# Kernel tuning notes

Measured on AMD Instinct MI355X. Metric: run time of the kernel, lower is better.

Reference implementation:

```python
import jax, jax.numpy as jnp
import numpy as np
import math

N = 50000
E = 1600000
A = 100          # num_atoms
H = 64           # hidden_dim / node_dim
L = 5            # num_layers
NB = 8           # num_basis
LMAX = 2
CUTOFF = 5.0


def setup_inputs() -> dict:
    key = jax.random.key(0)
    ks = jax.random.split(key, 32)
    s = 0.05
    inp = {
        'atomic_numbers': jax.random.randint(ks[0], (N,), 0, A),
        'pos': jax.random.normal(ks[1], (N, 3), jnp.float32) * 2.0,
        'edge_index': jax.random.randint(ks[2], (2, E), 0, N),
        # GaussianBasis widths
        'widths': jnp.ones((NB,), jnp.float32) * 0.5,
        # node embedding
        'embed': jax.random.normal(ks[3], (A, H), jnp.float32),
        # per-layer params, stacked on leading layer dim
        'rad_w1': jax.random.normal(ks[4], (L, NB, H), jnp.float32) * s,
        'rad_b1': jnp.zeros((L, H), jnp.float32),
        'rad_w2': jax.random.normal(ks[5], (L, H, H * (LMAX + 1)), jnp.float32) * s,
        'rad_b2': jnp.zeros((L, H * (LMAX + 1)), jnp.float32),
        'self_w': jax.random.normal(ks[6], (L, H, H), jnp.float32) * s,
        'self_b': jnp.zeros((L, H), jnp.float32),
        'proj_w': jax.random.normal(ks[7], (L, 2 * H, H), jnp.float32) * s,
        'proj_b': jnp.zeros((L, H), jnp.float32),
        'mlp_w1': jax.random.normal(ks[8], (L, H, 2 * H), jnp.float32) * s,
        'mlp_b1': jnp.zeros((L, 2 * H), jnp.float32),
        'mlp_w2': jax.random.normal(ks[9], (L, 2 * H, H), jnp.float32) * s,
        'mlp_b2': jnp.zeros((L, H), jnp.float32),
        'ln_g': jnp.ones((L, H), jnp.float32),
        'ln_b': jnp.zeros((L, H), jnp.float32),
        # readout MLP
        'ro_w1': jax.random.normal(ks[10], (H, H), jnp.float32) * s,
        'ro_b1': jnp.zeros((H,), jnp.float32),
        'ro_w2': jax.random.normal(ks[11], (H, H // 2), jnp.float32) * s,
        'ro_b2': jnp.zeros((H // 2,), jnp.float32),
        'ro_w3': jax.random.normal(ks[12], (H // 2, 1), jnp.float32) * s,
        'ro_b3': jnp.zeros((1,), jnp.float32),
        # per-species reference energies
        'atomic_e': jax.random.normal(ks[13], (A, 1), jnp.float32) * s,
    }
    return inp


def _layer_norm(x, g, b, eps=1e-5):
    mu = jnp.mean(x, axis=-1, keepdims=True)
    var = jnp.var(x, axis=-1, keepdims=True)
    return (x - mu) * jax.lax.rsqrt(var + eps) * g + b


def _spherical_harmonics(edge_vec):
    # real SH up to lmax=2, [E, 9] (computed for fidelity; unused by conv math)
    r = jnp.clip(jnp.linalg.norm(edge_vec, axis=-1), 1e-8, None)
    x, y, z = edge_vec[:, 0] / r, edge_vec[:, 1] / r, edge_vec[:, 2] / r
    x2, y2, z2 = x * x, y * y, z * z
    return jnp.stack([
        jnp.full_like(x, 0.28209479177387814),
        -0.4886025119029199 * y, 0.4886025119029199 * z, -0.4886025119029199 * x,
        1.0925484305920792 * x * y, -1.0925484305920792 * y * z,
        0.94617469575756 * z2 - 0.31539156525252 * (x2 + y2),
        -1.0925484305920792 * x * z, 0.5462742152960396 * (x2 - y2),
    ], axis=-1)


def _forward(atomic_numbers, pos, edge_index, widths, embed,
             rad_w1, rad_b1, rad_w2, rad_b2, self_w, self_b, proj_w, proj_b,
             mlp_w1, mlp_b1, mlp_w2, mlp_b2, ln_g, ln_b,
             ro_w1, ro_b1, ro_w2, ro_b2, ro_w3, ro_b3, atomic_e):
    n = pos.shape[0]
    row, col = edge_index[0], edge_index[1]
    edge_vec = pos[col] - pos[row]                          # [E,3]
    edge_len = jnp.linalg.norm(edge_vec, axis=-1, keepdims=True)  # [E,1]

    # GaussianBasis
    xr = edge_len / CUTOFF
    cut = 0.5 * (jnp.cos(xr * math.pi) + 1.0)
    cut = cut * (edge_len < CUTOFF).astype(jnp.float32)     # [E,1]
    centers = jnp.linspace(0.0, CUTOFF, NB)
    diff = edge_len - centers                               # [E,NB]
    edge_rbf = jnp.exp(-0.5 * (diff / jnp.clip(widths, 0.1, None)) ** 2) * cut

    edge_sh = _spherical_harmonics(edge_vec)  # computed but unused, as in source

    feats = embed[atomic_numbers]                           # [N,H]
    for i in range(L):
        # radial net -> per-edge weights [E, H*(lmax+1)]
        w = jax.nn.silu(edge_rbf @ rad_w1[i] + rad_b1[i]) @ rad_w2[i] + rad_b2[i]
        # messages: node_j[:,:,None] * w.view(E,H,lmax+1) summed over last dim
        # == node_j * w.reshape(E,H,lmax+1).sum(-1)
        wsum = w.reshape(-1, H, LMAX + 1).sum(axis=-1)      # [E,H]
        messages = feats[col] * wsum                        # gather + multiply
        agg = jax.ops.segment_sum(messages, row, num_segments=n)  # scatter-add
        self_out = feats @ self_w[i] + self_b[i]
        conv_out = jnp.concatenate([self_out, agg], axis=-1) @ proj_w[i] + proj_b[i]
        upd = jax.nn.silu(conv_out @ mlp_w1[i] + mlp_b1[i]) @ mlp_w2[i] + mlp_b2[i]
        feats = _layer_norm(feats + upd, ln_g[i], ln_b[i])

    h = jax.nn.silu(feats @ ro_w1 + ro_b1)
    h = jax.nn.silu(h @ ro_w2 + ro_b2)
    atomic_energies = h @ ro_w3 + ro_b3                     # [N,1]
    atomic_energies = atomic_energies + atomic_e[atomic_numbers]
    return atomic_energies.sum()                            # batch=None path


def reference(atomic_numbers, pos, edge_index, widths, embed,
              rad_w1, rad_b1, rad_w2, rad_b2, self_w, self_b, proj_w, proj_b,
              mlp_w1, mlp_b1, mlp_w2, mlp_b2, ln_g, ln_b,
              ro_w1, ro_b1, ro_w2, ro_b2, ro_w3, ro_b3, atomic_e):
    return _forward(atomic_numbers, pos, edge_index, widths, embed,
                    rad_w1, rad_b1, rad_w2, rad_b2, self_w, self_b, proj_w, proj_b,
                    mlp_w1, mlp_b1, mlp_w2, mlp_b2, ln_g, ln_b,
                    ro_w1, ro_b1, ro_w2, ro_b2, ro_w3, ro_b3, atomic_e)
```

## Files before the change

### kernel.cpp

```cpp
#include <hip/hip_runtime.h>
#include <hip/hip_fp16.h>
#include <math.h>

constexpr int N_NODES = 50000;
constexpr int N_EDGES = 1600000;
constexpr int HDIM    = 64;
constexpr int NLAYER  = 5;
constexpr int NBASIS  = 8;
constexpr int TLUT    = 256;
constexpr float CUT_R = 5.0f;
constexpr float PI_F  = 3.14159265358979f;

constexpr int NBKT = 196;
constexpr int BCAP = 9216;
constexpr int TILE = 2048;

typedef __attribute__((ext_vector_type(8))) short short8;
typedef __attribute__((ext_vector_type(4))) float f32x4;
#define MFMA16 __builtin_amdgcn_mfma_f32_16x16x32_bf16

__device__ __forceinline__ float siluf(float x) { return x / (1.0f + __expf(-x)); }

__device__ __forceinline__ unsigned int f2bf(float x) {
    unsigned int b = __float_as_uint(x);
    return (b + 0x7fffu + ((b >> 16) & 1u)) >> 16;
}
__device__ __forceinline__ float bf_lo(unsigned int u) { return __uint_as_float(u << 16); }
__device__ __forceinline__ float bf_hi(unsigned int u) { return __uint_as_float(u & 0xffff0000u); }

__device__ __forceinline__ unsigned int f2e5(float x) {
    unsigned short b = __half_as_ushort(__float2half(x));
    return ((unsigned int)b + 0x7Fu + ((b >> 8) & 1u)) >> 8;
}

__device__ __forceinline__ __half2 u2h2(unsigned int u) {
    union { unsigned int u; __half2 h; } x; x.u = u; return x.h;
}
__device__ __forceinline__ unsigned int h2u(__half2 h) {
    union { __half2 h; unsigned int u; } x; x.h = h; return x.u;
}

__device__ __forceinline__ int blockScan256Excl(int cv, int tid, int* wtot) {
    int v = cv;
    int lane = tid & 63;
    #pragma unroll
    for (int off = 1; off < 64; off <<= 1) {
        int t = __shfl_up(v, off, 64);
        if (lane >= off) v += t;
    }
    if (lane == 63) wtot[tid >> 6] = v;
    __syncthreads();
    int pre = 0;
    #pragma unroll
    for (int w = 0; w < 4; ++w)
        if (w < (tid >> 6)) pre += wtot[w];
    __syncthreads();
    return v + pre - cv;
}


__global__ void k_embed(const int* __restrict__ an, const float* __restrict__ embed,
                        unsigned short* __restrict__ featsbf,
                        unsigned char* __restrict__ featsf8) {
    int i = blockIdx.x * blockDim.x + threadIdx.x;
    if (i >= N_NODES * HDIM) return;
    int node = i >> 6, h = i & 63;
    float v = embed[an[node] * HDIM + h];
    featsbf[i] = (unsigned short)f2bf(v);
    featsf8[i] = (unsigned char)f2e5(v);
}

__global__ void k_edge(const int* __restrict__ row, const int* __restrict__ col,
                       const float* __restrict__ pos,
                       unsigned int* __restrict__ rec4, unsigned char* __restrict__ bkt) {
    int e = blockIdx.x * blockDim.x + threadIdx.x;
    if (e >= N_EDGES) return;
    int r = row[e], c = col[e];
    float dx = pos[c * 3 + 0] - pos[r * 3 + 0];
    float dy = pos[c * 3 + 1] - pos[r * 3 + 1];
    float dz = pos[c * 3 + 2] - pos[r * 3 + 2];
    float len = sqrtf(dx * dx + dy * dy + dz * dz);
    float t = len * ((float)(TLUT - 1) / CUT_R);
    t = fminf(t, (float)(TLUT - 1));
    unsigned int nn = (unsigned int)(t + 0.5f);
    if (nn > TLUT - 1) nn = TLUT - 1;
    rec4[e] = ((unsigned int)c << 16) | (nn << 8) | ((unsigned int)r & 255u);
    bkt[e]  = (unsigned char)(r >> 8);
}

__global__ __launch_bounds__(256) void k_binA(const unsigned int* __restrict__ rec4,
                                              const unsigned char* __restrict__ bkt,
                                              int* __restrict__ btail,
                                              unsigned int* __restrict__ binned) {
    __shared__ unsigned int ent[TILE];
    __shared__ short bb[TILE];
    __shared__ unsigned int sorted[TILE];
    __shared__ short sortedB[TILE];
    __shared__ int cnt[256], cnt2[256], base[256], gbase[256];
    __shared__ int wtot[4];
    const int tid = threadIdx.x;
    const int t0  = blockIdx.x * TILE;
    const int nv  = min(TILE, N_EDGES - t0);

    cnt[tid] = 0;
    __syncthreads();

    #pragma unroll
    for (int i = 0; i < TILE / 256; ++i) {
        int idx = i * 256 + tid;
        if (idx < nv) {
            ent[idx] = rec4[t0 + idx];
            int b = bkt[t0 + idx];
            bb[idx] = (short)b;
            atomicAdd(&cnt[b], 1);
        }
    }
    __syncthreads();
    int cv = cnt[tid];
    int excl = blockScan256Excl(cv, tid, wtot);
    base[tid] = excl;
    if (tid < NBKT && cv > 0) gbase[tid] = atomicAdd(&btail[tid], cv);
    cnt2[tid] = excl;
    __syncthreads();
    #pragma unroll
    for (int i = 0; i < TILE / 256; ++i) {
        int idx = i * 256 + tid;
        if (idx < nv) {
            int b = bb[idx];
            int p = atomicAdd(&cnt2[b], 1);
            sorted[p]  = ent[idx];
            sortedB[p] = (short)b;
        }
    }
    __syncthreads();
    for (int s = tid; s < nv; s += 256) {
        int b = sortedB[s];
        binned[(size_t)b * BCAP + gbase[b] + (s - base[b])] = sorted[s];
    }
}

__global__ void k_scanB(const int* __restrict__ btail, int* __restrict__ bbase) {
    __shared__ int wtot[4];
    int t = threadIdx.x;
    int v = (t < NBKT) ? btail[t] : 0;
    int excl = blockScan256Excl(v, t, wtot);
    if (t < NBKT) bbase[t] = excl;
}

__global__ __launch_bounds__(256) void k_binB(const unsigned int* __restrict__ binned,
                                              const int* __restrict__ btail,
                                              const int* __restrict__ bbase,
                                              int* __restrict__ starts,
                                              unsigned int* __restrict__ erec) {
    __shared__ int hist[256];
    __shared__ int cur[256];
    __shared__ int wtot[4];
    const int b = blockIdx.x;
    const int node0 = b << 8;
    const int t = threadIdx.x;
    hist[t] = 0;
    __syncthreads();
    const int cnt = btail[b];
    const unsigned int* src = binned + (size_t)b * BCAP;
    for (int s = t; s < cnt; s += 256)
        atomicAdd(&hist[src[s] & 255u], 1);
    __syncthreads();
    int h = hist[t];
    int excl = bbase[b] + blockScan256Excl(h, t, wtot);
    int n = node0 + t;
    if (n < N_NODES) starts[n] = excl;
    if (b == 0 && t == 0) starts[N_NODES] = N_EDGES;
    cur[t] = excl;
    __syncthreads();
    for (int s = t; s < cnt; s += 256) {
        unsigned int p = src[s];
        int pp = atomicAdd(&cur[p & 255u], 1);
        erec[pp] = p;
    }
}

__global__ void k_prep(const float* __restrict__ rad_w2, const float* __restrict__ self_w,
                       const float* __restrict__ proj_w,
                       const float* __restrict__ rad_b2, const float* __restrict__ self_b,
                       const float* __restrict__ proj_b,
                       float* __restrict__ W2s, float* __restrict__ Wsp,
                       float* __restrict__ b2s, float* __restrict__ bsp) {
    int i = blockIdx.x * blockDim.x + threadIdx.x;
    if (i < NLAYER * HDIM * HDIM) {
        int l = i / (HDIM * HDIM); int rem = i % (HDIM * HDIM);
        int k = rem / HDIM; int h = rem % HDIM;
        const float* w = rad_w2 + ((size_t)l * HDIM + k) * (HDIM * 3) + h * 3;
        W2s[i] = w[0] + w[1] + w[2];
        const float* sw = self_w + ((size_t)l * HDIM + k) * HDIM;
        const float* pw = proj_w + (size_t)l * 2 * HDIM * HDIM;
        float acc = 0.f;
        for (int m = 0; m < HDIM; ++m) acc += sw[m] * pw[m * HDIM + h];
        Wsp[i] = acc;
    } else {
        int i2 = i - NLAYER * HDIM * HDIM;
        if (i2 >= NLAYER * HDIM) return;
        int l = i2 / HDIM, h = i2 % HDIM;
        const float* rb2 = rad_b2 + l * HDIM * 3 + h * 3;
        b2s[i2] = rb2[0] + rb2[1] + rb2[2];
        float acc = proj_b[l * HDIM + h];
        const float* pw = proj_w + (size_t)l * 2 * HDIM * HDIM;
        const float* sb = self_b + l * HDIM;
        for (int m = 0; m < HDIM; ++m) acc += sb[m] * pw[m * HDIM + h];
        bsp[i2] = acc;
    }
}

__global__ void k_wtr(const float* __restrict__ Wsp, const float* __restrict__ proj_w,
                      const float* __restrict__ mlp_w1, const float* __restrict__ mlp_w2,
                      const float* __restrict__ ro_w1, const float* __restrict__ ro_w2,
                      unsigned short* __restrict__ WspT, unsigned short* __restrict__ PbT,
                      unsigned short* __restrict__ W1T, unsigned short* __restrict__ W2T,
                      unsigned short* __restrict__ Ro1T, unsigned short* __restrict__ Ro2T) {
    int i = blockIdx.x * blockDim.x + threadIdx.x;
    if (i < NLAYER * 24576) {
        int l = i / 24576, off = i % 24576;
        if (off < 4096) {
            int n = off >> 6, k = off & 63;
            WspT[(size_t)l * 4096 + off] = (unsigned short)f2bf(Wsp[(size_t)l * 4096 + k * 64 + n]);
        } else if (off < 8192) {
            int o = off - 4096; int n = o >> 6, k = o & 63;
            PbT[(size_t)l * 4096 + o] =
                (unsigned short)f2bf(proj_w[(size_t)l * 8192 + (64 + k) * 64 + n]);
        } else if (off < 16384) {
            int o = off - 8192; int n = o >> 6, k = o & 63;
            W1T[(size_t)l * 8192 + o] = (unsigned short)f2bf(mlp_w1[(size_t)l * 8192 + k * 128 + n]);
        } else {
            int o = off - 16384; int n = o >> 7, k = o & 127;
            W2T[(size_t)l * 8192 + o] = (unsigned short)f2bf(mlp_w2[(size_t)l * 8192 + k * 64 + n]);
        }
    } else {
        int i2 = i - NLAYER * 24576;
        if (i2 >= 6144) return;
        if (i2 < 4096) {
            int n = i2 >> 6, k = i2 & 63;
            Ro1T[i2] = (unsigned short)f2bf(ro_w1[k * 64 + n]);
        } else {
            int o = i2 - 4096; int n = o >> 6, k = o & 63;
            Ro2T[o] = (unsigned short)f2bf(ro_w2[k * 32 + n]);
        }
    }
}

__global__ void k_lut(const float* __restrict__ widths, const float* __restrict__ rad_w1,
                      const float* __restrict__ rad_b1, const float* __restrict__ W2s,
                      const float* __restrict__ b2s, unsigned short* __restrict__ lutH) {
    int bid = blockIdx.x;
    int l = bid / TLUT, t = bid % TLUT;
    int h = threadIdx.x;
    __shared__ float h1s[HDIM];
    float len = (float)t * (CUT_R / (float)(TLUT - 1));
    float cut = 0.0f;
    if (len < CUT_R) cut = 0.5f * (cosf(len * (PI_F / CUT_R)) + 1.0f);
    float acc = rad_b1[l * HDIM + h];
    for (int b = 0; b < NBASIS; ++b) {
        float wb = fmaxf(widths[b], 0.1f);
        float center = (float)b * (CUT_R / (float)(NBASIS - 1));
        float d = (len - center) / wb;
        float rbf = __expf(-0.5f * d * d) * cut;
        acc += rbf * rad_w1[(l * NBASIS + b) * HDIM + h];
    }
    h1s[h] = siluf(acc);
    __syncthreads();
    float o = b2s[l * HDIM + h];
    const float* w2 = W2s + (size_t)l * HDIM * HDIM;
    for (int k = 0; k < HDIM; ++k) o += h1s[k] * w2[k * HDIM + h];
    int m = h & 7;
    int pos = (h & ~7) | (m & 4) | ((m & 1) << 1) | ((m >> 1) & 1);
    lutH[(size_t)bid * HDIM + pos] = __half_as_ushort(__float2half(o));
}


__global__ __launch_bounds__(256) void k_agg(const uint2* __restrict__ featsf8_2,
                                             const uint4* __restrict__ lutH4_l,
                                             const int* __restrict__ starts,
                                             const unsigned int* __restrict__ erec,
                                             uint4* __restrict__ aggbf4) {
    int wid  = (blockIdx.x * blockDim.x + threadIdx.x) >> 6;
    int lane = threadIdx.x & 63;
    int slot = lane >> 3;
    int j    = lane & 7;
    if (wid >= N_NODES) return;
    int e0 = starts[wid], e1 = starts[wid + 1];
    __half2 a02 = u2h2(0u), a13 = u2h2(0u), a46 = u2h2(0u), a57 = u2h2(0u);
    #pragma unroll 2
    for (int e = e0 + slot; e < e1; e += 8) {
        unsigned int rec = erec[e];
        int c  = rec >> 16;
        int i0 = (rec >> 8) & 255;
        uint4 qw = lutH4_l[i0 * 8 + j];
        uint2 fb = featsf8_2[(size_t)c * 8 + j];
        a02 = __hfma2(u2h2((fb.x << 8) & 0xFF00FF00u), u2h2(qw.x), a02);
        a13 = __hfma2(u2h2(fb.x & 0xFF00FF00u),        u2h2(qw.y), a13);
        a46 = __hfma2(u2h2((fb.y << 8) & 0xFF00FF00u), u2h2(qw.z), a46);
        a57 = __hfma2(u2h2(fb.y & 0xFF00FF00u),        u2h2(qw.w), a57);
    }
    #pragma unroll
    for (int off = 8; off < 64; off <<= 1) {
        a02 = __hadd2(a02, u2h2((unsigned int)__shfl_xor((int)h2u(a02), off, 64)));
        a13 = __hadd2(a13, u2h2((unsigned int)__shfl_xor((int)h2u(a13), off, 64)));
        a46 = __hadd2(a46, u2h2((unsigned int)__shfl_xor((int)h2u(a46), off, 64)));
        a57 = __hadd2(a57, u2h2((unsigned int)__shfl_xor((int)h2u(a57), off, 64)));
    }
    if (slot == 0) {
        float c0 = __low2float(a02), c2 = __high2float(a02);
        float c1 = __low2float(a13), c3 = __high2float(a13);
        float c4 = __low2float(a46), c6 = __high2float(a46);
        float c5 = __low2float(a57), c7 = __high2float(a57);
        uint4 o;
        o.x = f2bf(c0) | (f2bf(c1) << 16);
        o.y = f2bf(c2) | (f2bf(c3) << 16);
        o.z = f2bf(c4) | (f2bf(c5) << 16);
        o.w = f2bf(c6) | (f2bf(c7) << 16);
        aggbf4[(size_t)wid * 8 + j] = o;
    }
}

constexpr int BP = 72;
template <bool FINAL>
__global__ __launch_bounds__(256) void k_node(
        unsigned short* __restrict__ featsbf,
        unsigned char* __restrict__ featsf8,
        const unsigned short* __restrict__ aggbf,
        const unsigned short* __restrict__ WspT_l, const unsigned short* __restrict__ PbT_l,
        const unsigned short* __restrict__ W1T_l, const unsigned short* __restrict__ W2T_l,
        const float* __restrict__ bsp_l,
        const float* __restrict__ mlp_b1_l, const float* __restrict__ mlp_b2_l,
        const float* __restrict__ ln_g_l, const float* __restrict__ ln_b_l,
        const int* __restrict__ an,
        const unsigned short* __restrict__ Ro1T, const unsigned short* __restrict__ Ro2T,
        const float* __restrict__ ro_b1, const float* __restrict__ ro_b2,
        const float* __restrict__ ro_w3, const float* __restrict__ ro_b3,
        const float* __restrict__ atomic_e, float* __restrict__ blockpart) {
    __shared__ unsigned short P[64 * BP];
    __shared__ unsigned short Q[64 * BP];
    __shared__ unsigned short S[64 * BP];
    const int tid  = threadIdx.x;
    const int lane = tid & 63;
    const int wib  = tid >> 6;
    const int mt   = __builtin_amdgcn_readfirstlane(wib);
    const int nb0  = blockIdx.x * 64;
    const int colL = lane & 15;
    const int kgrp = lane >> 4;

    #pragma unroll 4
    for (int i = 0; i < 16; ++i) {
        int r  = wib + i * 4;
        int nd = nb0 + r; nd = (nd < N_NODES) ? nd : (N_NODES - 1);
        P[r * BP + lane] = featsbf[(size_t)nd * 64 + lane];
        Q[r * BP + lane] = aggbf[(size_t)nd * 64 + lane];
    }
    __syncthreads();

    float xres[4][4];
    #pragma unroll
    for (int j = 0; j < 4; ++j)
        #pragma unroll
        for (int nt = 0; nt < 4; ++nt)
            xres[nt][j] = bf_lo(P[(mt * 16 + kgrp * 4 + j) * BP + nt * 16 + colL]);

    f32x4 acc[4];
    #pragma unroll
    for (int nt = 0; nt < 4; ++nt) {
        float b = bsp_l[nt * 16 + colL];
        acc[nt][0] = b; acc[nt][1] = b; acc[nt][2] = b; acc[nt][3] = b;
    }
    #pragma unroll
    for (int kb = 0; kb < 2; ++kb) {
        short8 ax = *(const short8*)&P[(mt * 16 + colL) * BP + kb * 32 + kgrp * 8];
        short8 aa = *(const short8*)&Q[(mt * 16 + colL) * BP + kb * 32 + kgrp * 8];
        #pragma unroll
        for (int nt = 0; nt < 4; ++nt) {
            short8 bw = *(const short8*)&WspT_l[(nt * 16 + colL) * 64 + kb * 32 + kgrp * 8];
            acc[nt] = MFMA16(ax, bw, acc[nt], 0, 0, 0);
            short8 bp = *(const short8*)&PbT_l[(nt * 16 + colL) * 64 + kb * 32 + kgrp * 8];
            acc[nt] = MFMA16(aa, bp, acc[nt], 0, 0, 0);
        }
    }
    __syncthreads();
    #pragma unroll
    for (int nt = 0; nt < 4; ++nt)
        #pragma unroll
        for (int j = 0; j < 4; ++j)
            P[(mt * 16 + kgrp * 4 + j) * BP + nt * 16 + colL] = (unsigned short)f2bf(acc[nt][j]);
    __syncthreads();

    {
        f32x4 m[8];
        #pragma unroll
        for (int nt = 0; nt < 8; ++nt) {
            float b = mlp_b1_l[nt * 16 + colL];
            m[nt][0] = b; m[nt][1] = b; m[nt][2] = b; m[nt][3] = b;
        }
        #pragma unroll
        for (int kb = 0; kb < 2; ++kb) {
            short8 ac = *(const short8*)&P[(mt * 16 + colL) * BP + kb * 32 + kgrp * 8];
            #pragma unroll
            for (int nt = 0; nt < 8; ++nt) {
                short8 bw = *(const short8*)&W1T_l[(nt * 16 + colL) * 64 + kb * 32 + kgrp * 8];
                m[nt] = MFMA16(ac, bw, m[nt], 0, 0, 0);
            }
        }
        __syncthreads();
        #pragma unroll
        for (int nt = 0; nt < 4; ++nt)
            #pragma unroll
            for (int j = 0; j < 4; ++j)
                Q[(mt * 16 + kgrp * 4 + j) * BP + nt * 16 + colL] =
                    (unsigned short)f2bf(siluf(m[nt][j]));
        #pragma unroll
        for (int nt = 4; nt < 8; ++nt)
            #pragma unroll
            for (int j = 0; j < 4; ++j)
                S[(mt * 16 + kgrp * 4 + j) * BP + (nt - 4) * 16 + colL] =
                    (unsigned short)f2bf(siluf(m[nt][j]));
    }
    __syncthreads();

    f32x4 u[4];
    #pragma unroll
    for (int nt = 0; nt < 4; ++nt) {
        float b = mlp_b2_l[nt * 16 + colL];
        u[nt][0] = b; u[nt][1] = b; u[nt][2] = b; u[nt][3] = b;
    }
    #pragma unroll
    for (int kb = 0; kb < 4; ++kb) {
        short8 am = (kb < 2)
            ? *(const short8*)&Q[(mt * 16 + colL) * BP + kb * 32 + kgrp * 8]
            : *(const short8*)&S[(mt * 16 + colL) * BP + (kb - 2) * 32 + kgrp * 8];
        #pragma unroll
        for (int nt = 0; nt < 4; ++nt) {
            short8 bw = *(const short8*)&W2T_l[(nt * 16 + colL) * 128 + kb * 32 + kgrp * 8];
            u[nt] = MFMA16(am, bw, u[nt], 0, 0, 0);
        }
    }

    float y[4][4];
    float s1[4] = {0, 0, 0, 0}, s2[4] = {0, 0, 0, 0};
    #pragma unroll
    for (int j = 0; j < 4; ++j) {
        #pragma unroll
        for (int nt = 0; nt < 4; ++nt) {
            float v = xres[nt][j] + u[nt][j];
            y[nt][j] = v;
            s1[j] += v; s2[j] += v * v;
        }
    }
    #pragma unroll
    for (int off = 1; off < 16; off <<= 1) {
        #pragma unroll
        for (int j = 0; j < 4; ++j) {
            s1[j] += __shfl_xor(s1[j], off, 64);
            s2[j] += __shfl_xor(s2[j], off, 64);
        }
    }
    float gv[4], bv[4];
    #pragma unroll
    for (int nt = 0; nt < 4; ++nt) {
        gv[nt] = ln_g_l[nt * 16 + colL];
        bv[nt] = ln_b_l[nt * 16 + colL];
    }
    if constexpr (!FINAL) {
        #pragma unroll
        for (int j = 0; j < 4; ++j) {
            int node = nb0 + mt * 16 + kgrp * 4 + j;
            if (node >= N_NODES) continue;
            float mu  = s1[j] * (1.0f / 64.0f);
            float var = s2[j] * (1.0f / 64.0f) - mu * mu;
            float rr  = rsqrtf(var + 1e-5f);
            #pragma unroll
            for (int nt = 0; nt < 4; ++nt) {
                float o = (y[nt][j] - mu) * rr * gv[nt] + bv[nt];
                size_t idx = (size_t)node * 64 + nt * 16 + colL;
                featsbf[idx] = (unsigned short)f2bf(o);
                featsf8[idx] = (unsigned char)f2e5(o);
            }
        }
    } else {
        __syncthreads();
        #pragma unroll
        for (int j = 0; j < 4; ++j) {
            float mu  = s1[j] * (1.0f / 64.0f);
            float var = s2[j] * (1.0f / 64.0f) - mu * mu;
            float rr  = rsqrtf(var + 1e-5f);
            #pragma unroll
            for (int nt = 0; nt < 4; ++nt) {
                float o = (y[nt][j] - mu) * rr * gv[nt] + bv[nt];
                P[(mt * 16 + kgrp * 4 + j) * BP + nt * 16 + colL] = (unsigned short)f2bf(o);
            }
        }
        __syncthreads();

        {
            f32x4 m[4];
            #pragma unroll
            for (int nt = 0; nt < 4; ++nt) {
                float b = ro_b1[nt * 16 + colL];
                m[nt][0] = b; m[nt][1] = b; m[nt][2] = b; m[nt][3] = b;
            }
            #pragma unroll
            for (int kb = 0; kb < 2; ++kb) {
                short8 ax = *(const short8*)&P[(mt * 16 + colL) * BP + kb * 32 + kgrp * 8];
                #pragma unroll
                for (int nt = 0; nt < 4; ++nt) {
                    short8 bw = *(const short8*)&Ro1T[(nt * 16 + colL) * 64 + kb * 32 + kgrp * 8];
                    m[nt] = MFMA16(ax, bw, m[nt], 0, 0, 0);
                }
            }
            __syncthreads();
            #pragma unroll
            for (int nt = 0; nt < 4; ++nt)
                #pragma unroll
                for (int j = 0; j < 4; ++j)
                    Q[(mt * 16 + kgrp * 4 + j) * BP + nt * 16 + colL] =
                        (unsigned short)f2bf(siluf(m[nt][j]));
        }
        __syncthreads();

        f32x4 uu[2];
        #pragma unroll
        for (int nt = 0; nt < 2; ++nt) {
            float b = ro_b2[nt * 16 + colL];
            uu[nt][0] = b; uu[nt][1] = b; uu[nt][2] = b; uu[nt][3] = b;
        }
        #pragma unroll
        for (int kb = 0; kb < 2; ++kb) {
            short8 am = *(const short8*)&Q[(mt * 16 + colL) * BP + kb * 32 + kgrp * 8];
            #pragma unroll
            for (int nt = 0; nt < 2; ++nt) {
                short8 bw = *(const short8*)&Ro2T[(nt * 16 + colL) * 64 + kb * 32 + kgrp * 8];
                uu[nt] = MFMA16(am, bw, uu[nt], 0, 0, 0);
            }
        }
        float w3[2];
        #pragma unroll
        for (int nt = 0; nt < 2; ++nt) w3[nt] = ro_w3[nt * 16 + colL];
        float part = 0.0f;
        #pragma unroll
        for (int j = 0; j < 4; ++j) {
            float c = siluf(uu[0][j]) * w3[0] + siluf(uu[1][j]) * w3[1];
            #pragma unroll
            for (int off = 1; off < 16; off <<= 1) c += __shfl_xor(c, off, 64);
            int node = nb0 + mt * 16 + kgrp * 4 + j;
            if (colL == 0 && node < N_NODES)
                part += c + ro_b3[0] + atomic_e[an[node]];
        }
        float* sred = (float*)S;
        sred[tid] = part;
        __syncthreads();
        for (int off = 128; off > 0; off >>= 1) {
            if (tid < off) sred[tid] += sred[tid + off];
            __syncthreads();
        }
        if (tid == 0) blockpart[blockIdx.x] = sred[0];
    }
}

__global__ void k_final(const float* __restrict__ blockpart, int nb, float* __restrict__ out) {
    __shared__ float s[256];
    float acc = 0.f;
    for (int i = threadIdx.x; i < nb; i += 256) acc += blockpart[i];
    s[threadIdx.x] = acc; __syncthreads();
    for (int off = 128; off > 0; off >>= 1) {
        if (threadIdx.x < off) s[threadIdx.x] += s[threadIdx.x + off];
        __syncthreads();
    }
    if (threadIdx.x == 0) out[0] = s[0];
}


extern "C" void kernel_launch(void* const* d_in, const int* in_sizes, int n_in,
                              void* d_out, int out_size, void* d_ws, size_t ws_size,
                              hipStream_t stream) {
    const int*   an       = (const int*)  d_in[0];
    const float* pos      = (const float*)d_in[1];
    const int*   edge     = (const int*)  d_in[2];
    const float* widths   = (const float*)d_in[3];
    const float* embed    = (const float*)d_in[4];
    const float* rad_w1   = (const float*)d_in[5];
    const float* rad_b1   = (const float*)d_in[6];
    const float* rad_w2   = (const float*)d_in[7];
    const float* rad_b2   = (const float*)d_in[8];
    const float* self_w   = (const float*)d_in[9];
    const float* self_b   = (const float*)d_in[10];
    const float* proj_w   = (const float*)d_in[11];
    const float* proj_b   = (const float*)d_in[12];
    const float* mlp_w1   = (const float*)d_in[13];
    const float* mlp_b1   = (const float*)d_in[14];
    const float* mlp_w2   = (const float*)d_in[15];
    const float* mlp_b2   = (const float*)d_in[16];
    const float* ln_g     = (const float*)d_in[17];
    const float* ln_b     = (const float*)d_in[18];
    const float* ro_w1    = (const float*)d_in[19];
    const float* ro_b1    = (const float*)d_in[20];
    const float* ro_w2    = (const float*)d_in[21];
    const float* ro_b2    = (const float*)d_in[22];
    const float* ro_w3    = (const float*)d_in[23];
    const float* ro_b3    = (const float*)d_in[24];
    const float* atomic_e = (const float*)d_in[25];

    char* w = (char*)d_ws;
    auto alloc = [&](size_t bytes) { char* p = w; w += (bytes + 255) & ~(size_t)255; return p; };
    unsigned short* featsbf = (unsigned short*)alloc(sizeof(unsigned short) * N_NODES * HDIM);
    unsigned char* featsf8  = (unsigned char*)alloc(sizeof(unsigned char) * N_NODES * HDIM);
    unsigned short* aggbf   = (unsigned short*)alloc(sizeof(unsigned short) * N_NODES * HDIM);
    unsigned short* lutH = (unsigned short*)alloc(sizeof(unsigned short) * NLAYER * TLUT * HDIM);
    float* W2s       = (float*)alloc(sizeof(float) * NLAYER * HDIM * HDIM);
    float* b2s       = (float*)alloc(sizeof(float) * NLAYER * HDIM);
    float* Wsp       = (float*)alloc(sizeof(float) * NLAYER * HDIM * HDIM);
    float* bsp       = (float*)alloc(sizeof(float) * NLAYER * HDIM);
    unsigned short* WspT = (unsigned short*)alloc(sizeof(unsigned short) * NLAYER * 4096);
    unsigned short* PbT  = (unsigned short*)alloc(sizeof(unsigned short) * NLAYER * 4096);
    unsigned short* W1T  = (unsigned short*)alloc(sizeof(unsigned short) * NLAYER * 8192);
    unsigned short* W2T  = (unsigned short*)alloc(sizeof(unsigned short) * NLAYER * 8192);
    unsigned short* Ro1T = (unsigned short*)alloc(sizeof(unsigned short) * 4096);
    unsigned short* Ro2T = (unsigned short*)alloc(sizeof(unsigned short) * 2048);
    unsigned int* erec = (unsigned int*)alloc(sizeof(unsigned int) * N_EDGES);
    unsigned int* rec4 = (unsigned int*)alloc(sizeof(unsigned int) * N_EDGES);
    unsigned char* bkt = (unsigned char*)alloc(sizeof(unsigned char) * N_EDGES);
    unsigned int* binned = (unsigned int*)alloc(sizeof(unsigned int) * (size_t)NBKT * BCAP);
    int*   btail     = (int*)  alloc(sizeof(int) * 256);
    int*   bbase     = (int*)  alloc(sizeof(int) * 256);
    int*   starts    = (int*)  alloc(sizeof(int) * (N_NODES + 1));
    float* blockpart = (float*)alloc(sizeof(float) * 1024);
    (void)ws_size; (void)in_sizes; (void)n_in; (void)out_size;

    const int* erow = edge;
    const int* ecol = edge + N_EDGES;

    hipMemsetAsync(btail, 0, sizeof(int) * 256, stream);
    k_embed<<<12500, 256, 0, stream>>>(an, embed, featsbf, featsf8);
    k_edge<<<(N_EDGES + 255) / 256, 256, 0, stream>>>(erow, ecol, pos, rec4, bkt);
    k_binA<<<(N_EDGES + TILE - 1) / TILE, 256, 0, stream>>>(rec4, bkt, btail, binned);
    k_scanB<<<1, 256, 0, stream>>>(btail, bbase);
    k_binB<<<NBKT, 256, 0, stream>>>(binned, btail, bbase, starts, erec);
    k_prep<<<(NLAYER * HDIM * HDIM + NLAYER * HDIM + 255) / 256, 256, 0, stream>>>(
        rad_w2, self_w, proj_w, rad_b2, self_b, proj_b, W2s, Wsp, b2s, bsp);
    k_wtr<<<(NLAYER * 24576 + 6144 + 255) / 256, 256, 0, stream>>>(
        Wsp, proj_w, mlp_w1, mlp_w2, ro_w1, ro_w2, WspT, PbT, W1T, W2T, Ro1T, Ro2T);
    k_lut<<<NLAYER * TLUT, 64, 0, stream>>>(widths, rad_w1, rad_b1, W2s, b2s, lutH);

    for (int l = 0; l < NLAYER; ++l) {
        k_agg<<<12500, 256, 0, stream>>>((const uint2*)featsf8,
                                         (const uint4*)(lutH + (size_t)l * TLUT * HDIM),
                                         starts, erec, (uint4*)aggbf);
        if (l < NLAYER - 1) {
            k_node<false><<<782, 256, 0, stream>>>(featsbf, featsf8, aggbf,
                WspT + (size_t)l * 4096, PbT + (size_t)l * 4096,
                W1T + (size_t)l * 8192, W2T + (size_t)l * 8192,
                bsp + l * HDIM, mlp_b1 + l * 2 * HDIM, mlp_b2 + l * HDIM,
                ln_g + l * HDIM, ln_b + l * HDIM,
                nullptr, nullptr, nullptr, nullptr, nullptr, nullptr, nullptr,
                nullptr, nullptr);
        } else {
            k_node<true><<<782, 256, 0, stream>>>(featsbf, featsf8, aggbf,
                WspT + (size_t)l * 4096, PbT + (size_t)l * 4096,
                W1T + (size_t)l * 8192, W2T + (size_t)l * 8192,
                bsp + l * HDIM, mlp_b1 + l * 2 * HDIM, mlp_b2 + l * HDIM,
                ln_g + l * HDIM, ln_b + l * HDIM,
                an, Ro1T, Ro2T, ro_b1, ro_b2, ro_w3, ro_b3, atomic_e, blockpart);
        }
    }

    k_final<<<1, 256, 0, stream>>>(blockpart, 782, (float*)d_out);
}
```

Baseline: 379.2 us.

## Merge embed/edge kernels, fold bucket scan into binB, vectorize node loads/stores

```diff
diff --git a/kernel.cpp b/kernel.cpp
--- a/kernel.cpp
+++ b/kernel.cpp
@@ -14,6 +14,7 @@
 constexpr int NBKT = 196;
 constexpr int BCAP = 9216;
 constexpr int TILE = 2048;
+constexpr int NBLK_EMBED = 12500;
 
 typedef __attribute__((ext_vector_type(8))) short short8;
 typedef __attribute__((ext_vector_type(4))) float f32x4;
@@ -26,7 +27,6 @@
     return (b + 0x7fffu + ((b >> 16) & 1u)) >> 16;
 }
 __device__ __forceinline__ float bf_lo(unsigned int u) { return __uint_as_float(u << 16); }
-__device__ __forceinline__ float bf_hi(unsigned int u) { return __uint_as_float(u & 0xffff0000u); }
 
 __device__ __forceinline__ unsigned int f2e5(float x) {
     unsigned short b = __half_as_ushort(__float2half(x));
@@ -59,33 +59,35 @@
 }
 
 
-__global__ void k_embed(const int* __restrict__ an, const float* __restrict__ embed,
-                        unsigned short* __restrict__ featsbf,
-                        unsigned char* __restrict__ featsf8) {
-    int i = blockIdx.x * blockDim.x + threadIdx.x;
-    if (i >= N_NODES * HDIM) return;
-    int node = i >> 6, h = i & 63;
-    float v = embed[an[node] * HDIM + h];
-    featsbf[i] = (unsigned short)f2bf(v);
-    featsf8[i] = (unsigned char)f2e5(v);
-}
-
-__global__ void k_edge(const int* __restrict__ row, const int* __restrict__ col,
+__global__ void k_init(const int* __restrict__ an, const float* __restrict__ embed,
+                       unsigned short* __restrict__ featsbf,
+                       unsigned char* __restrict__ featsf8,
+                       const int* __restrict__ row, const int* __restrict__ col,
                        const float* __restrict__ pos,
                        unsigned int* __restrict__ rec4, unsigned char* __restrict__ bkt) {
-    int e = blockIdx.x * blockDim.x + threadIdx.x;
-    if (e >= N_EDGES) return;
-    int r = row[e], c = col[e];
-    float dx = pos[c * 3 + 0] - pos[r * 3 + 0];
-    float dy = pos[c * 3 + 1] - pos[r * 3 + 1];
-    float dz = pos[c * 3 + 2] - pos[r * 3 + 2];
-    float len = sqrtf(dx * dx + dy * dy + dz * dz);
-    float t = len * ((float)(TLUT - 1) / CUT_R);
-    t = fminf(t, (float)(TLUT - 1));
-    unsigned int nn = (unsigned int)(t + 0.5f);
-    if (nn > TLUT - 1) nn = TLUT - 1;
-    rec4[e] = ((unsigned int)c << 16) | (nn << 8) | ((unsigned int)r & 255u);
-    bkt[e]  = (unsigned char)(r >> 8);
+    int b = blockIdx.x;
+    if (b < NBLK_EMBED) {
+        int i = b * 256 + threadIdx.x;
+        if (i >= N_NODES * HDIM) return;
+        int node = i >> 6, h = i & 63;
+        float v = embed[an[node] * HDIM + h];
+        featsbf[i] = (unsigned short)f2bf(v);
+        featsf8[i] = (unsigned char)f2e5(v);
+    } else {
+        int e = (b - NBLK_EMBED) * 256 + threadIdx.x;
+        if (e >= N_EDGES) return;
+        int r = row[e], c = col[e];
+        float dx = pos[c * 3 + 0] - pos[r * 3 + 0];
+        float dy = pos[c * 3 + 1] - pos[r * 3 + 1];
+        float dz = pos[c * 3 + 2] - pos[r * 3 + 2];
+        float len = sqrtf(dx * dx + dy * dy + dz * dz);
+        float t = len * ((float)(TLUT - 1) / CUT_R);
+        t = fminf(t, (float)(TLUT - 1));
+        unsigned int nn = (unsigned int)(t + 0.5f);
+        if (nn > TLUT - 1) nn = TLUT - 1;
+        rec4[e] = ((unsigned int)c << 16) | (nn << 8) | ((unsigned int)r & 255u);
+        bkt[e]  = (unsigned char)(r >> 8);
+    }
 }
 
 __global__ __launch_bounds__(256) void k_binA(const unsigned int* __restrict__ rec4,
@@ -139,34 +141,34 @@
     }
 }
 
-__global__ void k_scanB(const int* __restrict__ btail, int* __restrict__ bbase) {
-    __shared__ int wtot[4];
-    int t = threadIdx.x;
-    int v = (t < NBKT) ? btail[t] : 0;
-    int excl = blockScan256Excl(v, t, wtot);
-    if (t < NBKT) bbase[t] = excl;
-}
-
 __global__ __launch_bounds__(256) void k_binB(const unsigned int* __restrict__ binned,
                                               const int* __restrict__ btail,
-                                              const int* __restrict__ bbase,
                                               int* __restrict__ starts,
                                               unsigned int* __restrict__ erec) {
     __shared__ int hist[256];
     __shared__ int cur[256];
+    __shared__ int red[256];
     __shared__ int wtot[4];
     const int b = blockIdx.x;
     const int node0 = b << 8;
     const int t = threadIdx.x;
+    int part = 0;
+    for (int i = t; i < b; i += 256) part += btail[i];
+    red[t] = part;
     hist[t] = 0;
     __syncthreads();
+    for (int off = 128; off > 0; off >>= 1) {
+        if (t < off) red[t] += red[t + off];
+        __syncthreads();
+    }
+    const int bb0 = red[0];
     const int cnt = btail[b];
     const unsigned int* src = binned + (size_t)b * BCAP;
     for (int s = t; s < cnt; s += 256)
         atomicAdd(&hist[src[s] & 255u], 1);
     __syncthreads();
     int h = hist[t];
-    int excl = bbase[b] + blockScan256Excl(h, t, wtot);
+    int excl = bb0 + blockScan256Excl(h, t, wtot);
     int n = node0 + t;
     if (n < N_NODES) starts[n] = excl;
     if (b == 0 && t == 0) starts[N_NODES] = N_EDGES;
@@ -347,12 +349,16 @@
     const int colL = lane & 15;
     const int kgrp = lane >> 4;
 
-    #pragma unroll 4
-    for (int i = 0; i < 16; ++i) {
-        int r  = wib + i * 4;
-        int nd = nb0 + r; nd = (nd < N_NODES) ? nd : (N_NODES - 1);
-        P[r * BP + lane] = featsbf[(size_t)nd * 64 + lane];
-        Q[r * BP + lane] = aggbf[(size_t)nd * 64 + lane];
+    {
+        const uint4* gP = (const uint4*)(featsbf + (size_t)nb0 * 64);
+        const uint4* gQ = (const uint4*)(aggbf  + (size_t)nb0 * 64);
+        #pragma unroll
+        for (int i = 0; i < 2; ++i) {
+            int g = i * 256 + tid;
+            int row = g >> 3, q = g & 7;
+            *(uint4*)&P[row * BP + q * 8] = gP[g];
+            *(uint4*)&Q[row * BP + q * 8] = gQ[g];
+        }
     }
     __syncthreads();
 
@@ -465,20 +471,35 @@
         bv[nt] = ln_b_l[nt * 16 + colL];
     }
     if constexpr (!FINAL) {
+        unsigned char* f8t = (unsigned char*)S;
+        __syncthreads();
         #pragma unroll
         for (int j = 0; j < 4; ++j) {
-            int node = nb0 + mt * 16 + kgrp * 4 + j;
-            if (node >= N_NODES) continue;
+            int rrow = mt * 16 + kgrp * 4 + j;
             float mu  = s1[j] * (1.0f / 64.0f);
             float var = s2[j] * (1.0f / 64.0f) - mu * mu;
             float rr  = rsqrtf(var + 1e-5f);
             #pragma unroll
             for (int nt = 0; nt < 4; ++nt) {
                 float o = (y[nt][j] - mu) * rr * gv[nt] + bv[nt];
-                size_t idx = (size_t)node * 64 + nt * 16 + colL;
-                featsbf[idx] = (unsigned short)f2bf(o);
-                featsf8[idx] = (unsigned char)f2e5(o);
+                P[rrow * BP + nt * 16 + colL] = (unsigned short)f2bf(o);
+                f8t[rrow * 80 + nt * 16 + colL] = (unsigned char)f2e5(o);
             }
+        }
+        __syncthreads();
+        #pragma unroll
+        for (int i = 0; i < 2; ++i) {
+            int g = i * 256 + tid;
+            int row = g >> 3, q = g & 7;
+            if (nb0 + row < N_NODES)
+                *(uint4*)(featsbf + (size_t)(nb0 + row) * 64 + q * 8) =
+                    *(const uint4*)&P[row * BP + q * 8];
+        }
+        {
+            int row = tid >> 2, q = tid & 3;
+            if (nb0 + row < N_NODES)
+                *(uint4*)(featsf8 + (size_t)(nb0 + row) * 64 + q * 16) =
+                    *(const uint4*)&f8t[row * 80 + q * 16];
         }
     } else {
         __syncthreads();
@@ -605,9 +626,9 @@
 
     char* w = (char*)d_ws;
     auto alloc = [&](size_t bytes) { char* p = w; w += (bytes + 255) & ~(size_t)255; return p; };
-    unsigned short* featsbf = (unsigned short*)alloc(sizeof(unsigned short) * N_NODES * HDIM);
-    unsigned char* featsf8  = (unsigned char*)alloc(sizeof(unsigned char) * N_NODES * HDIM);
-    unsigned short* aggbf   = (unsigned short*)alloc(sizeof(unsigned short) * N_NODES * HDIM);
+    unsigned short* featsbf = (unsigned short*)alloc(sizeof(unsigned short) * (N_NODES + 64) * HDIM);
+    unsigned char* featsf8  = (unsigned char*)alloc(sizeof(unsigned char) * (N_NODES + 64) * HDIM);
+    unsigned short* aggbf   = (unsigned short*)alloc(sizeof(unsigned short) * (N_NODES + 64) * HDIM);
     unsigned short* lutH = (unsigned short*)alloc(sizeof(unsigned short) * NLAYER * TLUT * HDIM);
     float* W2s       = (float*)alloc(sizeof(float) * NLAYER * HDIM * HDIM);
     float* b2s       = (float*)alloc(sizeof(float) * NLAYER * HDIM);
@@ -624,7 +645,6 @@
     unsigned char* bkt = (unsigned char*)alloc(sizeof(unsigned char) * N_EDGES);
     unsigned int* binned = (unsigned int*)alloc(sizeof(unsigned int) * (size_t)NBKT * BCAP);
     int*   btail     = (int*)  alloc(sizeof(int) * 256);
-    int*   bbase     = (int*)  alloc(sizeof(int) * 256);
     int*   starts    = (int*)  alloc(sizeof(int) * (N_NODES + 1));
     float* blockpart = (float*)alloc(sizeof(float) * 1024);
     (void)ws_size; (void)in_sizes; (void)n_in; (void)out_size;
@@ -633,11 +653,10 @@
     const int* ecol = edge + N_EDGES;
 
     hipMemsetAsync(btail, 0, sizeof(int) * 256, stream);
-    k_embed<<<12500, 256, 0, stream>>>(an, embed, featsbf, featsf8);
-    k_edge<<<(N_EDGES + 255) / 256, 256, 0, stream>>>(erow, ecol, pos, rec4, bkt);
+    k_init<<<NBLK_EMBED + (N_EDGES + 255) / 256, 256, 0, stream>>>(
+        an, embed, featsbf, featsf8, erow, ecol, pos, rec4, bkt);
     k_binA<<<(N_EDGES + TILE - 1) / TILE, 256, 0, stream>>>(rec4, bkt, btail, binned);
-    k_scanB<<<1, 256, 0, stream>>>(btail, bbase);
-    k_binB<<<NBKT, 256, 0, stream>>>(binned, btail, bbase, starts, erec);
+    k_binB<<<NBKT, 256, 0, stream>>>(binned, btail, starts, erec);
     k_prep<<<(NLAYER * HDIM * HDIM + NLAYER * HDIM + 255) / 256, 256, 0, stream>>>(
         rad_w2, self_w, proj_w, rad_b2, self_b, proj_b, W2s, Wsp, b2s, bsp);
     k_wtr<<<(NLAYER * 24576 + 6144 + 255) / 256, 256, 0, stream>>>(
```

After: 375.2 us. No clear change (-1.1%).
